# Kernel tuning notes

Measured on AMD Instinct MI355X. Metric: run time of the kernel, lower is better.

## Reference

```python
import jax, jax.numpy as jnp
import numpy as np

N_NODES = 50000
N_EDGES = 800000
IN_DIM = 128
HIDDEN = 128
N_GRAPHS = 512


def setup_inputs() -> dict:
    key = jax.random.key(0)
    ks = jax.random.split(key, 9)
    x = jax.random.normal(ks[0], (N_NODES, IN_DIM), dtype=jnp.float32)
    edge_index = jax.random.randint(ks[1], (2, N_EDGES), 0, N_NODES, dtype=jnp.int32)
    batch = jnp.sort(jax.random.randint(ks[2], (N_NODES,), 0, N_GRAPHS, dtype=jnp.int32))
    # GCNConv params: linear (no bias) applied before propagation, bias added after.
    s1 = 1.0 / np.sqrt(IN_DIM)
    s2 = 1.0 / np.sqrt(HIDDEN)
    W1 = jax.random.uniform(ks[3], (IN_DIM, HIDDEN), jnp.float32, -s1, s1)
    b1 = jnp.zeros((HIDDEN,), jnp.float32)
    W2 = jax.random.uniform(ks[4], (HIDDEN, HIDDEN), jnp.float32, -s2, s2)
    b2 = jnp.zeros((HIDDEN,), jnp.float32)
    Wl = jax.random.uniform(ks[5], (HIDDEN, 1), jnp.float32, -s2, s2)
    bl = jax.random.uniform(ks[6], (1,), jnp.float32, -s2, s2)
    return {"x": x, "edge_index": edge_index, "batch": batch,
            "W1": W1, "b1": b1, "W2": W2, "b2": b2, "Wl": Wl, "bl": bl}


def gcn_conv(x, W, b, src, dst):
    # PyG GCNConv: h = D^{-1/2} (A + I) D^{-1/2} (x W) + b, with self-loops.
    h = x @ W                                        # [N, H]
    deg = jnp.zeros((N_NODES,), h.dtype).at[dst].add(1.0) + 1.0  # +1 for self-loop
    dinv = jax.lax.rsqrt(deg)                        # [N]
    msg = h[src] * (dinv[src] * dinv[dst])[:, None]  # [E, H] gather + normalize
    agg = jax.ops.segment_sum(msg, dst, num_segments=N_NODES)    # scatter-add
    agg = agg + h * (dinv * dinv)[:, None]           # self-loop contribution
    return agg + b


def reference(x, edge_index, batch, W1, b1, W2, b2, Wl, bl):
    src, dst = edge_index[0], edge_index[1]
    h = jax.nn.relu(gcn_conv(x, W1, b1, src, dst))
    h = jax.nn.relu(gcn_conv(h, W2, b2, src, dst))
    # global mean pool over graphs
    sums = jax.ops.segment_sum(h, batch, num_segments=N_GRAPHS)  # [G, H]
    cnt = jax.ops.segment_sum(jnp.ones((N_NODES,), h.dtype), batch, num_segments=N_GRAPHS)
    pooled = sums / jnp.maximum(cnt, 1.0)[:, None]
    return pooled @ Wl + bl
```

## Files before the change

kernel.cpp:

```cpp
#include <hip/hip_runtime.h>
#include <hip/hip_bf16.h>

#define N_NODES 50000
#define N_EDGES 800000
#define DIM 128
#define N_GRAPHS 512
#define NBUCK ((N_NODES + 63) / 64)
#define SC_CH 16384

typedef unsigned int uint;
typedef unsigned short ushort;
typedef __attribute__((ext_vector_type(8))) short short8;
typedef __attribute__((ext_vector_type(4))) float f32x4;

__device__ __forceinline__ ushort f2bf(float f) {
    uint u = __float_as_uint(f);
    uint r = (u + 0x7FFF + ((u >> 16) & 1)) >> 16;
    return (ushort)r;
}
__device__ __forceinline__ float bf2f(ushort h) {
    return __uint_as_float(((uint)h) << 16);
}
__device__ __forceinline__ uint pack2(float a, float b) {
    return (uint)f2bf(a) | ((uint)f2bf(b) << 16);
}
__device__ __forceinline__ float2 unpack2(uint v) {
    return make_float2(__uint_as_float(v << 16), __uint_as_float(v & 0xFFFF0000u));
}


__global__ void k_zero(int* __restrict__ p, int n) {
    int i = blockIdx.x * 256 + threadIdx.x;
    if (i < n) p[i] = 0;
}


__global__ __launch_bounds__(1024) void k_bcount(const int* __restrict__ ei,
                                                 int* __restrict__ bucketCnt, int E) {
    __shared__ int h[NBUCK];
    int tid = threadIdx.x;
    for (int t = tid; t < NBUCK; t += 1024) h[t] = 0;
    __syncthreads();
    for (int e = blockIdx.x * 1024 + tid; e < E; e += gridDim.x * 1024)
        atomicAdd(&h[ei[E + e] >> 6], 1);
    __syncthreads();
    for (int t = tid; t < NBUCK; t += 1024) {
        int c = h[t];
        if (c) atomicAdd(&bucketCnt[t], c);
    }
}

__global__ __launch_bounds__(1024) void k_bscan(const int* __restrict__ bucketCnt,
                                                int* __restrict__ bucketStart,
                                                int* __restrict__ bucketCursor) {
    __shared__ int wsum[16];
    int tid = threadIdx.x;
    int lane = tid & 63, wv = tid >> 6;
    int v = (tid < NBUCK) ? bucketCnt[tid] : 0;
    int s = v;
    #pragma unroll
    for (int off = 1; off < 64; off <<= 1) {
        int u = __shfl_up(s, off, 64);
        if (lane >= off) s += u;
    }
    if (lane == 63) wsum[wv] = s;
    __syncthreads();
    int woff = 0;
    #pragma unroll
    for (int w = 0; w < 16; ++w) woff += (w < wv) ? wsum[w] : 0;
    int excl = woff + s - v;
    if (tid < NBUCK) {
        bucketStart[tid] = excl;
        bucketCursor[tid] = excl;
    }
    if (tid == 1023) {
        int tot = 0;
        #pragma unroll
        for (int w = 0; w < 16; ++w) tot += wsum[w];
        bucketStart[NBUCK] = tot;
    }
}

__global__ __launch_bounds__(1024) void k_bscatter(const int* __restrict__ ei,
                                                   int* __restrict__ bucketCursor,
                                                   uint2* __restrict__ epair, int E) {
    __shared__ int hc[NBUCK];
    __shared__ int hbase[NBUCK];
    int tid = threadIdx.x;
    int e0 = blockIdx.x * SC_CH;
    int e1 = min(e0 + SC_CH, E);
    for (int t = tid; t < NBUCK; t += 1024) hc[t] = 0;
    __syncthreads();
    for (int e = e0 + tid; e < e1; e += 1024)
        atomicAdd(&hc[ei[E + e] >> 6], 1);
    __syncthreads();
    for (int t = tid; t < NBUCK; t += 1024) {
        int c = hc[t];
        hbase[t] = c ? atomicAdd(&bucketCursor[t], c) : 0;
        hc[t] = 0;
    }
    __syncthreads();
    for (int e = e0 + tid; e < e1; e += 1024) {
        int s = ei[e], d = ei[E + e];
        int b = d >> 6;
        int off = atomicAdd(&hc[b], 1);
        epair[hbase[b] + off] = make_uint2((uint)s, (uint)d);
    }
}

__global__ __launch_bounds__(256) void k_localcsr(const uint2* __restrict__ epair,
                                                  const int* __restrict__ bucketStart,
                                                  int* __restrict__ rowStart,
                                                  float* __restrict__ dinv,
                                                  int* __restrict__ csr) {
    __shared__ int cnt[64];
    __shared__ int cur[64];
    int tid = threadIdx.x;
    int b = blockIdx.x;
    int b0 = b << 6;
    int s = bucketStart[b], e = bucketStart[b + 1];
    if (tid < 64) cnt[tid] = 0;
    __syncthreads();
    for (int i = s + tid; i < e; i += 256)
        atomicAdd(&cnt[epair[i].y - b0], 1);
    __syncthreads();
    if (tid < 64) {
        int c = cnt[tid];
        int sc = c;
        #pragma unroll
        for (int off = 1; off < 64; off <<= 1) {
            int u = __shfl_up(sc, off, 64);
            if (tid >= off) sc += u;
        }
        int excl = sc - c;
        int node = b0 + tid;
        if (node < N_NODES) {
            rowStart[node] = s + excl;
            dinv[node] = rsqrtf((float)c + 1.0f);
        }
        cur[tid] = s + excl;
    }
    if (tid == 0 && b == NBUCK - 1) rowStart[N_NODES] = e;
    __syncthreads();
    for (int i = s + tid; i < e; i += 256) {
        uint2 p = epair[i];
        int pos = atomicAdd(&cur[p.y - b0], 1);
        csr[pos] = (int)p.x;
    }
}


__global__ __launch_bounds__(256) void k_wconv(const float* __restrict__ W1,
                                               const float* __restrict__ W2,
                                               uint* __restrict__ wf1,
                                               uint* __restrict__ wf2) {
    int t = blockIdx.x * 256 + threadIdx.x;
    const float* W = (t < 8192) ? W1 : W2;
    uint* dst = (t < 8192) ? wf1 : wf2;
    int r = t & 8191;
    int j2 = r & 3;
    int lane = (r >> 2) & 63;
    int tk = r >> 8;
    int kc = tk & 3, ct = tk >> 2;
    int j = j2 * 2;
    int k = kc * 32 + (lane >> 4) * 8 + j;
    int n = ct * 16 + (lane & 15);
    dst[r] = pack2(W[k * 128 + n], W[(k + 1) * 128 + n]);
}


template<bool BF16IN>
__global__ __launch_bounds__(256) void k_lin_mfma(const void* __restrict__ Xv,
                                                  const uint* __restrict__ Wfrag,
                                                  const float* __restrict__ dinv,
                                                  uint* __restrict__ out, int N) {
    int wv = threadIdx.x >> 6, lane = threadIdx.x & 63;
    int strip = blockIdx.x * 4 + wv;
    int row0 = strip * 16;
    if (row0 >= N) return;
    int m = lane & 15;
    int kg = lane >> 4;
    int arow = row0 + m;
    bool valid = arow < N;

    short8 af[4];
    if constexpr (!BF16IN) {
        const float* X = (const float*)Xv;
        const float* base = X + (size_t)arow * DIM + kg * 8;
        #pragma unroll
        for (int kc = 0; kc < 4; ++kc) {
            float4 a0 = make_float4(0.f, 0.f, 0.f, 0.f), a1 = a0;
            if (valid) {
                a0 = *(const float4*)(base + kc * 32);
                a1 = *(const float4*)(base + kc * 32 + 4);
            }
            short8 f;
            f[0] = (short)f2bf(a0.x); f[1] = (short)f2bf(a0.y);
            f[2] = (short)f2bf(a0.z); f[3] = (short)f2bf(a0.w);
            f[4] = (short)f2bf(a1.x); f[5] = (short)f2bf(a1.y);
            f[6] = (short)f2bf(a1.z); f[7] = (short)f2bf(a1.w);
            af[kc] = f;
        }
    } else {
        const uint* X = (const uint*)Xv;
        const uint* base = X + (size_t)arow * 64 + kg * 4;
        #pragma unroll
        for (int kc = 0; kc < 4; ++kc) {
            union { uint4 u; short8 s; } cv;
            cv.u = valid ? *(const uint4*)(base + kc * 16) : make_uint4(0, 0, 0, 0);
            af[kc] = cv.s;
        }
    }

    f32x4 acc[8];
    #pragma unroll
    for (int ct = 0; ct < 8; ++ct) acc[ct] = (f32x4){0.f, 0.f, 0.f, 0.f};

    #pragma unroll
    for (int ct = 0; ct < 8; ++ct) {
        #pragma unroll
        for (int kc = 0; kc < 4; ++kc) {
            union { uint4 u; short8 s; } bv;
            bv.u = *(const uint4*)(Wfrag + ((size_t)(ct * 4 + kc) * 64 + lane) * 4);
            acc[ct] = __builtin_amdgcn_mfma_f32_16x16x32_bf16(af[kc], bv.s, acc[ct], 0, 0, 0);
        }
    }

    ushort* ob = (ushort*)out;
    #pragma unroll
    for (int reg = 0; reg < 4; ++reg) {
        int orow = row0 + kg * 4 + reg;
        if (orow < N) {
            float di = dinv[orow];
            size_t rb = (size_t)orow * DIM + m;
            #pragma unroll
            for (int ct = 0; ct < 8; ++ct)
                ob[rb + ct * 16] = f2bf(acc[ct][reg] * di);
        }
    }
}


template<bool FUSE_HEAD>
__global__ __launch_bounds__(256) void k_aggregate(const uint* __restrict__ HS,
                                                   const int* __restrict__ rowStart,
                                                   const int* __restrict__ csr,
                                                   const float* __restrict__ dinv,
                                                   const float* __restrict__ bias,
                                                   const float* __restrict__ Wl,
                                                   uint* __restrict__ outRow,
                                                   float* __restrict__ outY, int n) {
    int wv = threadIdx.x >> 6, lane = threadIdx.x & 63;
    int nid = blockIdx.x * 4 + wv;
    if (nid >= n) return;
    uint sv = HS[(size_t)nid * 64 + lane];
    float2 acc = unpack2(sv);
    int beg = rowStart[nid], end = rowStart[nid + 1];
    int e = beg;
    for (; e + 3 < end; e += 4) {
        int s0 = csr[e], s1 = csr[e + 1], s2 = csr[e + 2], s3 = csr[e + 3];
        uint v0 = HS[(size_t)s0 * 64 + lane];
        uint v1 = HS[(size_t)s1 * 64 + lane];
        uint v2 = HS[(size_t)s2 * 64 + lane];
        uint v3 = HS[(size_t)s3 * 64 + lane];
        float2 f0 = unpack2(v0), f1 = unpack2(v1), f2 = unpack2(v2), f3 = unpack2(v3);
        acc.x += (f0.x + f1.x) + (f2.x + f3.x);
        acc.y += (f0.y + f1.y) + (f2.y + f3.y);
    }
    for (; e < end; ++e) {
        uint v0 = HS[(size_t)csr[e] * 64 + lane];
        float2 f0 = unpack2(v0);
        acc.x += f0.x;
        acc.y += f0.y;
    }
    float di = dinv[nid];
    int c = lane * 2;
    float ox = fmaxf(acc.x * di + bias[c], 0.f);
    float oy = fmaxf(acc.y * di + bias[c + 1], 0.f);
    if constexpr (!FUSE_HEAD) {
        outRow[(size_t)nid * 64 + lane] = pack2(ox, oy);
    } else {
        float part = ox * Wl[c] + oy * Wl[c + 1];
        #pragma unroll
        for (int off = 32; off > 0; off >>= 1) part += __shfl_down(part, off, 64);
        if (lane == 0) outY[nid] = part;
    }
}


__global__ __launch_bounds__(64) void k_pool_y(const float* __restrict__ y,
                                               const int* __restrict__ batch,
                                               const float* __restrict__ bl,
                                               float* __restrict__ out, int n) {
    int g = blockIdx.x;
    int lane = threadIdx.x;
    int lo = 0, hi = n;
    while (lo < hi) { int mid = (lo + hi) >> 1; if (batch[mid] < g) lo = mid + 1; else hi = mid; }
    int s = lo;
    hi = n;
    while (lo < hi) { int mid = (lo + hi) >> 1; if (batch[mid] < g + 1) lo = mid + 1; else hi = mid; }
    int e = lo;

    float sum = 0.f;
    for (int i = s + lane; i < e; i += 64) sum += y[i];
    #pragma unroll
    for (int off = 32; off > 0; off >>= 1) sum += __shfl_down(sum, off, 64);
    if (lane == 0) out[g] = sum / fmaxf((float)(e - s), 1.0f) + bl[0];
}


extern "C" void kernel_launch(void* const* d_in, const int* in_sizes, int n_in,
                              void* d_out, int out_size, void* d_ws, size_t ws_size,
                              hipStream_t stream) {
    const float* x  = (const float*)d_in[0];
    const int*   ei = (const int*)d_in[1];
    const int*   batch = (const int*)d_in[2];
    const float* W1 = (const float*)d_in[3];
    const float* b1 = (const float*)d_in[4];
    const float* W2 = (const float*)d_in[5];
    const float* b2 = (const float*)d_in[6];
    const float* Wl = (const float*)d_in[7];
    const float* bl = (const float*)d_in[8];
    float* out = (float*)d_out;

    uint* hs  = (uint*)d_ws;
    uint* h2b = hs + (size_t)N_NODES * 64;
    float* dinv = (float*)(h2b + (size_t)N_NODES * 64);
    float* ynode = dinv + N_NODES;
    int* rowStart = (int*)(ynode + N_NODES);
    int* bucketCnt = rowStart + N_NODES + 4;
    int* bucketStart = bucketCnt + 784;
    int* bucketCursor = bucketStart + 784;
    int* csr = bucketCursor + 784;
    uint2* epair = (uint2*)(csr + N_EDGES);
    uint* wf1 = (uint*)(epair + N_EDGES);
    uint* wf2 = wf1 + 8192;

    k_wconv<<<64, 256, 0, stream>>>(W1, W2, wf1, wf2);

    k_zero<<<(NBUCK + 255) / 256, 256, 0, stream>>>(bucketCnt, NBUCK);
    k_bcount<<<64, 1024, 0, stream>>>(ei, bucketCnt, N_EDGES);
    k_bscan<<<1, 1024, 0, stream>>>(bucketCnt, bucketStart, bucketCursor);
    k_bscatter<<<(N_EDGES + SC_CH - 1) / SC_CH, 1024, 0, stream>>>(ei, bucketCursor, epair, N_EDGES);
    k_localcsr<<<NBUCK, 256, 0, stream>>>(epair, bucketStart, rowStart, dinv, csr);

    int strips = (N_NODES + 15) / 16;
    int gemmGrid = (strips + 3) / 4;
    int aggGrid  = (N_NODES + 3) / 4;

    k_lin_mfma<false><<<gemmGrid, 256, 0, stream>>>(x, wf1, dinv, hs, N_NODES);
    k_aggregate<false><<<aggGrid, 256, 0, stream>>>(hs, rowStart, csr, dinv, b1, Wl, h2b, ynode, N_NODES);

    k_lin_mfma<true><<<gemmGrid, 256, 0, stream>>>(h2b, wf2, dinv, hs, N_NODES);
    k_aggregate<true><<<aggGrid, 256, 0, stream>>>(hs, rowStart, csr, dinv, b2, Wl, h2b, ynode, N_NODES);

    k_pool_y<<<N_GRAPHS, 64, 0, stream>>>(ynode, batch, bl, out, N_NODES);
}
```

Baseline: 165.2 us.

## Split feature matrix into column panels and aggregate per panel with 4 edge groups

Stores the bf16 hidden features as four 32-column panels, each node row 64 bytes. Aggregation now runs a 2D grid over nodes and panels, with the four 16-lane groups of a wave each walking every fourth edge, then reduces across groups with shuffles. The aim is a smaller gather footprint per panel, for better cache locality, and more edges in flight per wave. The change also packs edge pairs into a single 32-bit word (source index in the low 16 bits, local destination above) and merges weight conversion with the bucket-count zeroing. The packing truncates source indices above 65535, which is unsafe for 50000 nodes only if the node count grows. The per-panel head partials are summed in the pool kernel.

```diff
diff --git a/kernel.cpp b/kernel.cpp
--- a/kernel.cpp
+++ b/kernel.cpp
@@ -13,14 +13,13 @@
 typedef __attribute__((ext_vector_type(8))) short short8;
 typedef __attribute__((ext_vector_type(4))) float f32x4;
 
+#define HSB_IDX(p, node, u) ((((size_t)(p) * N_NODES) + (node)) * 16 + (u))
+
 __device__ __forceinline__ ushort f2bf(float f) {
     uint u = __float_as_uint(f);
     uint r = (u + 0x7FFF + ((u >> 16) & 1)) >> 16;
     return (ushort)r;
 }
-__device__ __forceinline__ float bf2f(ushort h) {
-    return __uint_as_float(((uint)h) << 16);
-}
 __device__ __forceinline__ uint pack2(float a, float b) {
     return (uint)f2bf(a) | ((uint)f2bf(b) << 16);
 }
@@ -29,9 +28,24 @@
 }
 
 
-__global__ void k_zero(int* __restrict__ p, int n) {
-    int i = blockIdx.x * 256 + threadIdx.x;
-    if (i < n) p[i] = 0;
+__global__ __launch_bounds__(256) void k_init(const float* __restrict__ W1,
+                                              const float* __restrict__ W2,
+                                              uint* __restrict__ wf1,
+                                              uint* __restrict__ wf2,
+                                              int* __restrict__ bucketCnt) {
+    int t = blockIdx.x * 256 + threadIdx.x;
+    if (t < NBUCK) bucketCnt[t] = 0;
+    const float* W = (t < 8192) ? W1 : W2;
+    uint* dst = (t < 8192) ? wf1 : wf2;
+    int r = t & 8191;
+    int j2 = r & 3;
+    int lane = (r >> 2) & 63;
+    int tk = r >> 8;
+    int kc = tk & 3, ct = tk >> 2;
+    int j = j2 * 2;
+    int k = kc * 32 + (lane >> 4) * 8 + j;
+    int n = ct * 16 + (lane & 15);
+    dst[r] = pack2(W[k * 128 + n], W[(k + 1) * 128 + n]);
 }
 
 
@@ -83,7 +97,7 @@
 
 __global__ __launch_bounds__(1024) void k_bscatter(const int* __restrict__ ei,
                                                    int* __restrict__ bucketCursor,
-                                                   uint2* __restrict__ epair, int E) {
+                                                   uint* __restrict__ epk, int E) {
     __shared__ int hc[NBUCK];
     __shared__ int hbase[NBUCK];
     int tid = threadIdx.x;
@@ -104,11 +118,11 @@
         int s = ei[e], d = ei[E + e];
         int b = d >> 6;
         int off = atomicAdd(&hc[b], 1);
-        epair[hbase[b] + off] = make_uint2((uint)s, (uint)d);
-    }
-}
-
-__global__ __launch_bounds__(256) void k_localcsr(const uint2* __restrict__ epair,
+        epk[hbase[b] + off] = (uint)s | ((uint)(d & 63) << 16);
+    }
+}
+
+__global__ __launch_bounds__(256) void k_localcsr(const uint* __restrict__ epk,
                                                   const int* __restrict__ bucketStart,
                                                   int* __restrict__ rowStart,
                                                   float* __restrict__ dinv,
@@ -122,7 +136,7 @@
     if (tid < 64) cnt[tid] = 0;
     __syncthreads();
     for (int i = s + tid; i < e; i += 256)
-        atomicAdd(&cnt[epair[i].y - b0], 1);
+        atomicAdd(&cnt[epk[i] >> 16], 1);
     __syncthreads();
     if (tid < 64) {
         int c = cnt[tid];
@@ -143,29 +157,10 @@
     if (tid == 0 && b == NBUCK - 1) rowStart[N_NODES] = e;
     __syncthreads();
     for (int i = s + tid; i < e; i += 256) {
-        uint2 p = epair[i];
-        int pos = atomicAdd(&cur[p.y - b0], 1);
-        csr[pos] = (int)p.x;
-    }
-}
-
-
-__global__ __launch_bounds__(256) void k_wconv(const float* __restrict__ W1,
-                                               const float* __restrict__ W2,
-                                               uint* __restrict__ wf1,
-                                               uint* __restrict__ wf2) {
-    int t = blockIdx.x * 256 + threadIdx.x;
-    const float* W = (t < 8192) ? W1 : W2;
-    uint* dst = (t < 8192) ? wf1 : wf2;
-    int r = t & 8191;
-    int j2 = r & 3;
-    int lane = (r >> 2) & 63;
-    int tk = r >> 8;
-    int kc = tk & 3, ct = tk >> 2;
-    int j = j2 * 2;
-    int k = kc * 32 + (lane >> 4) * 8 + j;
-    int n = ct * 16 + (lane & 15);
-    dst[r] = pack2(W[k * 128 + n], W[(k + 1) * 128 + n]);
+        uint p = epk[i];
+        int pos = atomicAdd(&cur[p >> 16], 1);
+        csr[pos] = (int)(p & 0xFFFFu);
+    }
 }
 
 
@@ -203,11 +198,11 @@
         }
     } else {
         const uint* X = (const uint*)Xv;
-        const uint* base = X + (size_t)arow * 64 + kg * 4;
         #pragma unroll
         for (int kc = 0; kc < 4; ++kc) {
             union { uint4 u; short8 s; } cv;
-            cv.u = valid ? *(const uint4*)(base + kc * 16) : make_uint4(0, 0, 0, 0);
+            cv.u = valid ? *(const uint4*)(X + HSB_IDX(kc, arow, kg * 4))
+                         : make_uint4(0, 0, 0, 0);
             af[kc] = cv.s;
         }
     }
@@ -232,10 +227,12 @@
         int orow = row0 + kg * 4 + reg;
         if (orow < N) {
             float di = dinv[orow];
-            size_t rb = (size_t)orow * DIM + m;
             #pragma unroll
-            for (int ct = 0; ct < 8; ++ct)
-                ob[rb + ct * 16] = f2bf(acc[ct][reg] * di);
+            for (int ct = 0; ct < 8; ++ct) {
+                int col = ct * 16 + m;
+                int p = col >> 5, cb = col & 31;
+                ob[((size_t)p * N_NODES + orow) * 32 + cb] = f2bf(acc[ct][reg] * di);
+            }
         }
     }
 }
@@ -253,37 +250,39 @@
     int wv = threadIdx.x >> 6, lane = threadIdx.x & 63;
     int nid = blockIdx.x * 4 + wv;
     if (nid >= n) return;
-    uint sv = HS[(size_t)nid * 64 + lane];
-    float2 acc = unpack2(sv);
+    int p = blockIdx.y;
+    int l16 = lane & 15, eg = lane >> 4;
+
+    float2 acc = make_float2(0.f, 0.f);
+    if (eg == 0) acc = unpack2(HS[HSB_IDX(p, nid, l16)]);
+
     int beg = rowStart[nid], end = rowStart[nid + 1];
-    int e = beg;
-    for (; e + 3 < end; e += 4) {
-        int s0 = csr[e], s1 = csr[e + 1], s2 = csr[e + 2], s3 = csr[e + 3];
-        uint v0 = HS[(size_t)s0 * 64 + lane];
-        uint v1 = HS[(size_t)s1 * 64 + lane];
-        uint v2 = HS[(size_t)s2 * 64 + lane];
-        uint v3 = HS[(size_t)s3 * 64 + lane];
-        float2 f0 = unpack2(v0), f1 = unpack2(v1), f2 = unpack2(v2), f3 = unpack2(v3);
-        acc.x += (f0.x + f1.x) + (f2.x + f3.x);
-        acc.y += (f0.y + f1.y) + (f2.y + f3.y);
-    }
-    for (; e < end; ++e) {
-        uint v0 = HS[(size_t)csr[e] * 64 + lane];
-        float2 f0 = unpack2(v0);
-        acc.x += f0.x;
-        acc.y += f0.y;
-    }
+    for (int e = beg + eg; e < end; e += 4) {
+        int src = csr[e];
+        float2 f = unpack2(HS[HSB_IDX(p, src, l16)]);
+        acc.x += f.x;
+        acc.y += f.y;
+    }
+    acc.x += __shfl_xor(acc.x, 16);
+    acc.y += __shfl_xor(acc.y, 16);
+    acc.x += __shfl_xor(acc.x, 32);
+    acc.y += __shfl_xor(acc.y, 32);
+
     float di = dinv[nid];
-    int c = lane * 2;
+    int c = p * 32 + l16 * 2;
     float ox = fmaxf(acc.x * di + bias[c], 0.f);
     float oy = fmaxf(acc.y * di + bias[c + 1], 0.f);
     if constexpr (!FUSE_HEAD) {
-        outRow[(size_t)nid * 64 + lane] = pack2(ox, oy);
+        if (eg == 0) outRow[HSB_IDX(p, nid, l16)] = pack2(ox, oy);
     } else {
         float part = ox * Wl[c] + oy * Wl[c + 1];
-        #pragma unroll
-        for (int off = 32; off > 0; off >>= 1) part += __shfl_down(part, off, 64);
-        if (lane == 0) outY[nid] = part;
+        if (eg == 0) {
+            part += __shfl_down(part, 8, 16);
+            part += __shfl_down(part, 4, 16);
+            part += __shfl_down(part, 2, 16);
+            part += __shfl_down(part, 1, 16);
+            if (l16 == 0) outY[(size_t)p * N_NODES + nid] = part;
+        }
     }
 }
 
@@ -302,7 +301,8 @@
     int e = lo;
 
     float sum = 0.f;
-    for (int i = s + lane; i < e; i += 64) sum += y[i];
+    for (int i = s + lane; i < e; i += 64)
+        sum += (y[i] + y[N_NODES + i]) + (y[2 * N_NODES + i] + y[3 * N_NODES + i]);
     #pragma unroll
     for (int off = 32; off > 0; off >>= 1) sum += __shfl_down(sum, off, 64);
     if (lane == 0) out[g] = sum / fmaxf((float)(e - s), 1.0f) + bl[0];
@@ -327,26 +327,25 @@
     uint* h2b = hs + (size_t)N_NODES * 64;
     float* dinv = (float*)(h2b + (size_t)N_NODES * 64);
     float* ynode = dinv + N_NODES;
-    int* rowStart = (int*)(ynode + N_NODES);
+    int* rowStart = (int*)(ynode + 4 * N_NODES);
     int* bucketCnt = rowStart + N_NODES + 4;
     int* bucketStart = bucketCnt + 784;
     int* bucketCursor = bucketStart + 784;
     int* csr = bucketCursor + 784;
-    uint2* epair = (uint2*)(csr + N_EDGES);
-    uint* wf1 = (uint*)(epair + N_EDGES);
+    uint* epk = (uint*)(csr + N_EDGES);
+    uint* wf1 = epk + N_EDGES;
     uint* wf2 = wf1 + 8192;
 
-    k_wconv<<<64, 256, 0, stream>>>(W1, W2, wf1, wf2);
-
-    k_zero<<<(NBUCK + 255) / 256, 256, 0, stream>>>(bucketCnt, NBUCK);
+    k_init<<<64, 256, 0, stream>>>(W1, W2, wf1, wf2, bucketCnt);
+
     k_bcount<<<64, 1024, 0, stream>>>(ei, bucketCnt, N_EDGES);
     k_bscan<<<1, 1024, 0, stream>>>(bucketCnt, bucketStart, bucketCursor);
-    k_bscatter<<<(N_EDGES + SC_CH - 1) / SC_CH, 1024, 0, stream>>>(ei, bucketCursor, epair, N_EDGES);
-    k_localcsr<<<NBUCK, 256, 0, stream>>>(epair, bucketStart, rowStart, dinv, csr);
+    k_bscatter<<<(N_EDGES + SC_CH - 1) / SC_CH, 1024, 0, stream>>>(ei, bucketCursor, epk, N_EDGES);
+    k_localcsr<<<NBUCK, 256, 0, stream>>>(epk, bucketStart, rowStart, dinv, csr);
 
     int strips = (N_NODES + 15) / 16;
     int gemmGrid = (strips + 3) / 4;
-    int aggGrid  = (N_NODES + 3) / 4;
+    dim3 aggGrid((N_NODES + 3) / 4, 4);
 
     k_lin_mfma<false><<<gemmGrid, 256, 0, stream>>>(x, wf1, dinv, hs, N_NODES);
     k_aggregate<false><<<aggGrid, 256, 0, stream>>>(hs, rowStart, csr, dinv, b1, Wl, h2b, ynode, N_NODES);
```

Result: slower. 287.6 us (+74.1%).
